# Kernel tuning notes

Measured on AMD Instinct MI355X. Metric: run time of the kernel, lower is better.

The kernel has to match this reference:

```python
import jax, jax.numpy as jnp
import numpy as np

IN_CH = 128
HID = 64
EPS = 1e-5
N_NODES = 20000
E_UND = 80000


def _build_line_graph(edge_index, num_nodes):
    # dedupe to unique undirected edges (src<dst); line-graph nodes = these edges
    src = np.asarray(edge_index[0]); dst = np.asarray(edge_index[1])
    m = src < dst
    u, v = src[m], dst[m]
    key = u.astype(np.int64) * num_nodes + v.astype(np.int64)
    _, first = np.unique(key, return_index=True)
    u, v = u[first], v[first]
    E = u.shape[0]
    # incidence lists grouped by node; all ordered pairs of co-incident edges
    nodes = np.concatenate([u, v])
    eids = np.concatenate([np.arange(E), np.arange(E)])
    order = np.argsort(nodes, kind="stable")
    nodes_s, eids_s = nodes[order], eids[order]
    counts = np.bincount(nodes_s, minlength=num_nodes)
    offsets = np.concatenate([np.zeros(1, np.int64), np.cumsum(counts)])
    grp_start = offsets[nodes_s]
    reps = counts[nodes_s]
    total = int(reps.sum())
    starts = np.cumsum(reps) - reps
    idx = np.arange(total) - np.repeat(starts, reps) + np.repeat(grp_start, reps)
    row = np.repeat(eids_s, reps); col = eids_s[idx]
    keep = row != col
    return np.stack([u, v]), np.stack([row[keep], col[keep]])


def _gcn_conv(x, src, dst, W, b):
    # PyG GCNConv: add self loops, symmetric D^-1/2 (A+I) D^-1/2 normalization
    N = x.shape[0]
    sl = jnp.arange(N)
    s = jnp.concatenate([src, sl]); d = jnp.concatenate([dst, sl])
    deg = jax.ops.segment_sum(jnp.ones(s.shape[0], x.dtype), d, num_segments=N)
    dinv = jax.lax.rsqrt(jnp.maximum(deg, 1.0))
    h = x @ W
    msg = h[s] * (dinv[s] * dinv[d])[:, None]
    return jax.ops.segment_sum(msg, d, num_segments=N) + b


def _edge_scores(line_x, lsrc, ldst, W1, b1, gamma1, beta1, W2, b2):
    h = _gcn_conv(line_x, lsrc, ldst, W1, b1)
    mu = h.mean(0); var = h.var(0)  # BatchNorm1d, training-mode batch stats
    h = jax.nn.relu(gamma1 * (h - mu) * jax.lax.rsqrt(var + EPS) + beta1)
    return jax.nn.sigmoid(_gcn_conv(h, lsrc, ldst, W2, b2))[:, 0]


def _cluster(clean, topk_idx, num_nodes):
    ti = np.asarray(topk_idx)
    sel_src = np.asarray(clean[0])[ti]; sel_dst = np.asarray(clean[1])[ti]
    n2c = np.arange(num_nodes)
    rev = sel_dst[::-1]
    _, fi = np.unique(rev, return_index=True)
    last = sel_dst.shape[0] - 1 - fi
    n2c[sel_dst[last]] = sel_src[last]
    uniq = np.unique(n2c)
    M = int(uniq.shape[0])
    old_to_new = np.full(num_nodes, -1, np.int64)
    old_to_new[uniq] = np.arange(M)
    return old_to_new[n2c], uniq, M


def _make_graph():
    rng = np.random.default_rng(0)
    a = rng.integers(0, N_NODES, E_UND)
    off = rng.integers(1, N_NODES, E_UND)
    b = (a + off) % N_NODES  # no self loops
    u = np.minimum(a, b); v = np.maximum(a, b)
    return np.stack([np.concatenate([u, v]), np.concatenate([v, u])]).astype(np.int64)


def _make_params():
    ks = jax.random.split(jax.random.key(0), 4)
    x = jax.random.normal(ks[0], (N_NODES, IN_CH), jnp.float32)
    W1 = jax.random.normal(ks[1], (IN_CH, HID), jnp.float32) / np.float32(np.sqrt(IN_CH))
    b1 = jnp.zeros((HID,), jnp.float32)
    gamma1 = jnp.ones((HID,), jnp.float32)
    beta1 = jnp.zeros((HID,), jnp.float32)
    W2 = jax.random.normal(ks[2], (HID, 1), jnp.float32) / np.float32(np.sqrt(HID))
    b2 = jnp.zeros((1,), jnp.float32)
    return x, W1, b1, gamma1, beta1, W2, b2


def setup_inputs() -> dict:
    x, W1, b1, gamma1, beta1, W2, b2 = _make_params()
    return {
        "x": x, "W1": W1, "b1": b1, "gamma1": gamma1, "beta1": beta1,
        "W2": W2, "b2": b2,
        "edge_index": jnp.asarray(_make_graph()),
        "batch": jnp.zeros((N_NODES,), jnp.int32),
    }


def reference(x, W1, b1, gamma1, beta1, W2, b2, edge_index, batch):
    N = x.shape[0]
    clean, line_ei = _build_line_graph(edge_index, N)
    csrc = jnp.asarray(clean[0]); cdst = jnp.asarray(clean[1])
    lsrc = jnp.asarray(line_ei[0]); ldst = jnp.asarray(line_ei[1])
    line_x = 0.5 * (x[csrc] + x[cdst])  # line-graph node features
    scores = _edge_scores(line_x, lsrc, ldst, W1, b1, gamma1, beta1, W2, b2)
    E_c = scores.shape[0]
    k = max(1, min(E_c // 2, N // 2))
    _, topk_idx = jax.lax.top_k(scores, k)
    new_indices, uniq, M = _cluster(clean, topk_idx, N)
    ni = jnp.asarray(new_indices)
    # aggregate: per-cluster mean of member node features (code's weights are unused)
    counts = jax.ops.segment_sum(jnp.ones(N, x.dtype), ni, num_segments=M)
    x_pool = jax.ops.segment_sum(x, ni, num_segments=M) / counts[:, None]
    batch_pool = batch[jnp.asarray(uniq)]
    # build_new_edges: relabel, drop self loops, coalesce (sorted unique)
    ei = np.asarray(edge_index)
    ns = new_indices[ei[0]]; nd = new_indices[ei[1]]
    keep = ns != nd
    pk = ns[keep] * M + nd[keep]
    upk = np.unique(pk)
    edge_index_pool = jnp.asarray(np.stack([upk // M, upk % M]))
    return (x_pool, edge_index_pool, batch_pool, scores, ni)
```

## Files before the change

kernel.cpp:

```cpp
#include <hip/hip_runtime.h>
#include <stdint.h>

typedef unsigned long long u64;
typedef unsigned int u32;

#define NND 20000
#define EUA 160000
#define EFE 80000
#define ICH 128
#define HIDC 64
#define SCAN_BS 256
#define NB_N ((NND + 255) / 256)
#define NB_EU ((EUA + 255) / 256)
#define NB_EF ((EFE + 255) / 256)
#define NB_E64 ((EFE * HIDC + 255) / 256)
#define NSCAN_B ((NND + SCAN_BS - 1) / SCAN_BS)
#define HIST_BLOCKS 128
#define GEB 64
#define XS_PAD 132
#define NCHAIN 4096
#define BK64 64
#define SEL_BINS 4096


__global__ void kScanA(const int* __restrict__ in, int* __restrict__ out,
                       int* __restrict__ bsums, int n) {
    __shared__ int sh[SCAN_BS];
    int tid = threadIdx.x;
    int i = blockIdx.x * SCAN_BS + tid;
    int v = (i < n) ? in[i] : 0;
    sh[tid] = v;
    __syncthreads();
    for (int o = 1; o < SCAN_BS; o <<= 1) {
        int t = (tid >= o) ? sh[tid - o] : 0;
        __syncthreads();
        sh[tid] += t;
        __syncthreads();
    }
    if (i < n) out[i] = sh[tid] - v;
    if (tid == SCAN_BS - 1) bsums[blockIdx.x] = sh[tid];
}
__global__ void kScanB(int* __restrict__ out, const int* __restrict__ bsums,
                       int n, int nb, int* __restrict__ totalDst) {
    __shared__ int sh[160];
    int tid = threadIdx.x;
    if (tid <= nb) sh[tid] = (tid < nb) ? bsums[tid] : 0;
    __syncthreads();
    if (tid == 0) {
        int acc = 0;
        for (int i = 0; i < nb; i++) { int t = sh[i]; sh[i] = acc; acc += t; }
        sh[nb] = acc;
    }
    __syncthreads();
    int i = blockIdx.x * SCAN_BS + tid;
    if (i < n) out[i] += sh[blockIdx.x];
    if (i == 0) {
        int tot = sh[nb];
        out[n] = tot;
        *totalDst = tot;
    }
}

__global__ void kFilterScatter64(const int* __restrict__ ei, int* __restrict__ cnt,
                                 int* __restrict__ bucketV) {
    int i = blockIdx.x * 256 + threadIdx.x;
    if (i >= EUA) return;
    int s = ei[i], d = ei[EUA + i];
    if (s < d) {
        int p = atomicAdd(&cnt[s], 1);
        bucketV[(s << 6) + p] = d;
    }
}
__global__ void kRankSort64(const int* __restrict__ in, int* __restrict__ out,
                            const int* __restrict__ lenA, int* __restrict__ ucnt) {
    int a = blockIdx.x;
    int len = lenA[a];
    int base = a << 6;
    for (int j = threadIdx.x; j < len; j += 64) {
        int v = in[base + j];
        int r = 0;
        for (int i = 0; i < len; i++) {
            int w = in[base + i];
            r += (w < v) || (w == v && i < j);
        }
        out[base + r] = v;
    }
    __syncthreads();
    int c = 0;
    for (int j = threadIdx.x; j < len; j += 64)
        c += (j == 0) || (out[base + j] != out[base + j - 1]);
#pragma unroll
    for (int o = 32; o > 0; o >>= 1) c += __shfl_down(c, o, 64);
    if (threadIdx.x == 0) ucnt[a] = c;
}
__global__ void kCompactInc(const int* __restrict__ arr, const int* __restrict__ cnt,
                            const int* __restrict__ uoff, int* __restrict__ eU,
                            int* __restrict__ eV, int* __restrict__ icnt) {
    int u = blockIdx.x * 256 + threadIdx.x;
    if (u >= NND) return;
    int s = u << 6, e = s + cnt[u], o = uoff[u];
    int myc = 0;
    for (int i = s; i < e; i++)
        if (i == s || arr[i] != arr[i - 1]) {
            int v = arr[i];
            eU[o] = u; eV[o] = v; o++;
            atomicAdd(&icnt[v], 1);
            myc++;
        }
    if (myc) atomicAdd(&icnt[u], myc);
}

__global__ void kIncScatterDinv64(const int* __restrict__ eU, const int* __restrict__ eV,
                                  const int* __restrict__ scal, int* __restrict__ itmp,
                                  int* __restrict__ ilist, const int* __restrict__ icnt,
                                  float* __restrict__ dinv) {
    int e = blockIdx.x * 256 + threadIdx.x;
    if (e >= scal[0]) return;
    int u = eU[e], v = eV[e];
    ilist[(u << 6) + atomicAdd(&itmp[u], 1)] = e;
    ilist[(v << 6) + atomicAdd(&itmp[v], 1)] = e;
    dinv[e] = rsqrtf((float)(icnt[u] + icnt[v] - 1));
}

__global__ void kGemm(const float* __restrict__ x, const float* __restrict__ W1,
                      const int* __restrict__ eU, const int* __restrict__ eV,
                      const int* __restrict__ scal, float* __restrict__ h) {
    __shared__ float W1s[ICH][HIDC];
    __shared__ float xs[GEB][XS_PAD];
    int t = threadIdx.x;
    int E = scal[0];
    int e0 = blockIdx.x * GEB;
    if (e0 >= E) return;

    {
        const float4* Wv = (const float4*)W1;
        float4* Ws = (float4*)&W1s[0][0];
        for (int i = t; i < ICH * HIDC / 4; i += 256) Ws[i] = Wv[i];
    }
    {
        int eb = t >> 2, q = t & 3;
        int e = e0 + eb;
        if (e < E) {
            int u = eU[e], v = eV[e];
            const float4* xu = (const float4*)(x + (size_t)u * ICH) + q * 8;
            const float4* xv = (const float4*)(x + (size_t)v * ICH) + q * 8;
            float* xd = &xs[eb][q * 32];
#pragma unroll
            for (int i = 0; i < 8; i++) {
                float4 a = xu[i], b = xv[i];
                xd[i * 4 + 0] = 0.5f * (a.x + b.x);
                xd[i * 4 + 1] = 0.5f * (a.y + b.y);
                xd[i * 4 + 2] = 0.5f * (a.z + b.z);
                xd[i * 4 + 3] = 0.5f * (a.w + b.w);
            }
        }
    }
    __syncthreads();

    int cg4 = (t & 15) * 4;
    int es = t >> 4;
    float a00=0,a01=0,a02=0,a03=0, a10=0,a11=0,a12=0,a13=0;
    float a20=0,a21=0,a22=0,a23=0, a30=0,a31=0,a32=0,a33=0;
#pragma unroll 4
    for (int k = 0; k < ICH; k++) {
        float4 wv = *(const float4*)&W1s[k][cg4];
        float x0 = xs[es][k], x1 = xs[es + 16][k];
        float x2 = xs[es + 32][k], x3 = xs[es + 48][k];
        a00 += x0 * wv.x; a01 += x0 * wv.y; a02 += x0 * wv.z; a03 += x0 * wv.w;
        a10 += x1 * wv.x; a11 += x1 * wv.y; a12 += x1 * wv.z; a13 += x1 * wv.w;
        a20 += x2 * wv.x; a21 += x2 * wv.y; a22 += x2 * wv.z; a23 += x2 * wv.w;
        a30 += x3 * wv.x; a31 += x3 * wv.y; a32 += x3 * wv.z; a33 += x3 * wv.w;
    }
    int e;
    e = e0 + es;
    if (e < E) *(float4*)&h[(size_t)e * HIDC + cg4] = make_float4(a00, a01, a02, a03);
    e = e0 + es + 16;
    if (e < E) *(float4*)&h[(size_t)e * HIDC + cg4] = make_float4(a10, a11, a12, a13);
    e = e0 + es + 32;
    if (e < E) *(float4*)&h[(size_t)e * HIDC + cg4] = make_float4(a20, a21, a22, a23);
    e = e0 + es + 48;
    if (e < E) *(float4*)&h[(size_t)e * HIDC + cg4] = make_float4(a30, a31, a32, a33);
}

__global__ void kSGather(const float* __restrict__ h, const float* __restrict__ dinv,
                         const int* __restrict__ icnt, const int* __restrict__ ilist,
                         float* __restrict__ S) {
    int n = blockIdx.x;
    int c = threadIdx.x;
    int base = n << 6, len = icnt[n];
    float acc = 0.f;
    for (int j = 0; j < len; j++) {
        int ed = ilist[base + j];
        acc += h[(size_t)ed * HIDC + c] * dinv[ed];
    }
    S[(size_t)n * HIDC + c] = acc;
}
__global__ void kConv1Red1(const float* __restrict__ h, const float* __restrict__ S,
                           const float* __restrict__ dinv, const int* __restrict__ eU,
                           const int* __restrict__ eV, const float* __restrict__ b1,
                           const int* __restrict__ scal, float* __restrict__ h2,
                           float* __restrict__ partial, float* __restrict__ partial2) {
    int t = threadIdx.x;
    int g = blockIdx.x * 4 + (t >> 6);
    int c = t & 63;
    int E = scal[0];
    float bc = b1[c];
    float acc = 0.f, acc2 = 0.f;
    for (int e = g; e < E; e += NCHAIN) {
        float a = dinv[e];
        float v = a * (S[(size_t)eU[e] * HIDC + c] + S[(size_t)eV[e] * HIDC + c]) -
                  a * a * h[(size_t)e * HIDC + c] + bc;
        h2[(size_t)e * HIDC + c] = v;
        acc += v;
        acc2 += v * v;
    }
    partial[g * HIDC + c] = acc;
    partial2[g * HIDC + c] = acc2;
}
__global__ void kRed2(const float* __restrict__ partial, const float* __restrict__ partial2,
                      const int* __restrict__ scal, float* __restrict__ muvar) {
    __shared__ float sh[4][HIDC];
    __shared__ float sh2[4][HIDC];
    int t = threadIdx.x;
    int q = t >> 6, c = t & 63;
    float acc = 0.f, acc2 = 0.f;
    int g0 = q * (NCHAIN / 4);
    for (int g = g0; g < g0 + NCHAIN / 4; g++) {
        acc += partial[g * HIDC + c];
        acc2 += partial2[g * HIDC + c];
    }
    sh[q][c] = acc;
    sh2[q][c] = acc2;
    __syncthreads();
    if (q == 0) {
        float Ef = (float)scal[0];
        float mu = (((sh[0][c] + sh[1][c]) + sh[2][c]) + sh[3][c]) / Ef;
        float m2 = (((sh2[0][c] + sh2[1][c]) + sh2[2][c]) + sh2[3][c]) / Ef;
        muvar[c] = mu;
        muvar[HIDC + c] = m2 - mu * mu;
    }
}
__global__ void kNormZ(const float* __restrict__ h2, const float* __restrict__ muvar,
                       const float* __restrict__ gamma1, const float* __restrict__ beta1,
                       const float* __restrict__ W2, const int* __restrict__ scal,
                       float* __restrict__ z) {
    int idx = blockIdx.x * 256 + threadIdx.x;
    int e = idx >> 6;
    if (e >= scal[0]) return;
    int c = idx & 63;
    float t = gamma1[c] * (h2[idx] - muvar[c]) * rsqrtf(muvar[HIDC + c] + 1e-5f) + beta1[c];
    t = t > 0.f ? t : 0.f;
    float p = t * W2[c];
#pragma unroll
    for (int o = 32; o > 0; o >>= 1) p += __shfl_down(p, o, 64);
    if (c == 0) z[e] = p;
}
__global__ void kS2(const float* __restrict__ z, const float* __restrict__ dinv,
                    const int* __restrict__ icnt, const int* __restrict__ ilist,
                    float* __restrict__ S2) {
    int n = blockIdx.x * 256 + threadIdx.x;
    if (n >= NND) return;
    int base = n << 6, len = icnt[n];
    float acc = 0.f;
    for (int j = 0; j < len; j++) {
        int e = ilist[base + j];
        acc += z[e] * dinv[e];
    }
    S2[n] = acc;
}
__global__ void kScore(const float* __restrict__ z, const float* __restrict__ S2,
                       const float* __restrict__ dinv, const int* __restrict__ eU,
                       const int* __restrict__ eV, const float* __restrict__ b2,
                       const int* __restrict__ scal, float* __restrict__ score,
                       u64* __restrict__ okey, u64* __restrict__ minOkey,
                       int* __restrict__ hist0) {
    __shared__ int sh[SEL_BINS];
    int t = threadIdx.x;
    for (int j = t; j < SEL_BINS; j += 256) sh[j] = 0;
    __syncthreads();
    int e = blockIdx.x * 256 + t;
    if (e < NND) minOkey[e] = ~0ULL;
    int E = scal[0];
    if (e < E) {
        float a = dinv[e];
        float l = a * (S2[eU[e]] + S2[eV[e]]) - a * a * z[e] + b2[0];
        float s = 1.f / (1.f + expf(-l));
        score[e] = s;
        u32 b = __float_as_uint(s);
        b = (b >> 31) ? ~b : (b | 0x80000000u);
        u64 key = (((u64)b) << 17) | (u32)(0x1FFFFu - (u32)e);
        okey[e] = key;
        atomicAdd(&sh[(int)((key >> 36) & (SEL_BINS - 1))], 1);
    }
    __syncthreads();
    for (int j = t; j < SEL_BINS; j += 256) {
        int v = sh[j];
        if (v) atomicAdd(&hist0[j], v);
    }
}

__device__ __forceinline__ u64 selReplay(const int* __restrict__ histBase, int passes,
                                         int E, int t, int* aux, int* shTmp) {
    int kr = E / 2;
    if (kr > NND / 2) kr = NND / 2;
    if (kr < 1) kr = 1;
    u64 pref = 1ULL << 48;
    for (int q = 0; q < passes; q++) {
        int shift = 36 - 12 * q;
        const int* hq = histBase + q * SEL_BINS;
        int b[16];
        int g = 0;
#pragma unroll
        for (int j = 0; j < 16; j++) { b[j] = hq[16 * t + j]; g += b[j]; }
        aux[t] = g;
        __syncthreads();
        for (int o = 1; o < 256; o <<= 1) {
            int v = (t + o < 256) ? aux[t + o] : 0;
            __syncthreads();
            aux[t] += v;
            __syncthreads();
        }
        int suf = aux[t] - g;
        if (suf < kr && kr <= suf + g) {
            int cum = suf, found = 16 * t;
            for (int j = 15; j >= 0; j--) {
                int hc = b[j];
                if (cum + hc >= kr) { found = 16 * t + j; break; }
                cum += hc;
            }
            shTmp[0] = found;
            shTmp[1] = kr - cum;
        }
        __syncthreads();
        pref |= ((u64)shTmp[0]) << shift;
        kr = shTmp[1];
        __syncthreads();
    }
    return pref;
}
__global__ void kHistR(const u64* __restrict__ okey, const int* __restrict__ scal,
                       int* __restrict__ histBase, int pass) {
    __shared__ int sh[4][SEL_BINS];
    __shared__ int aux[256];
    __shared__ int shTmp[2];
    int t = threadIdx.x;
    int E = scal[0];
    u64 p = selReplay(histBase, pass, E, t, aux, shTmp);
    for (int j = t; j < 4 * SEL_BINS; j += 256) ((int*)sh)[j] = 0;
    __syncthreads();
    int wv = t >> 6;
    int shift = 36 - 12 * pass;
    u64 maskHi = (~0ULL) << (shift + 12);
    for (int e = blockIdx.x * 256 + t; e < E; e += HIST_BLOCKS * 256) {
        u64 kk = okey[e];
        if ((kk & maskHi) == p)
            atomicAdd(&sh[wv][(int)((kk >> shift) & (SEL_BINS - 1))], 1);
    }
    __syncthreads();
    int* hp = histBase + pass * SEL_BINS;
    for (int j = t; j < SEL_BINS; j += 256) {
        int v = sh[0][j] + sh[1][j] + sh[2][j] + sh[3][j];
        if (v) atomicAdd(&hp[j], v);
    }
}

__global__ void kMinKey(const u64* __restrict__ okey, const int* __restrict__ eV,
                        const int* __restrict__ scal, const int* __restrict__ histBase,
                        u64* __restrict__ minOkey) {
    __shared__ int aux[256];
    __shared__ int shTmp[2];
    int t = threadIdx.x;
    int E = scal[0];
    u64 pref = selReplay(histBase, 4, E, t, aux, shTmp);
    int i = blockIdx.x * 256 + t;
    if (i < E) {
        u64 k = okey[i];
        if (k >= pref) atomicMin(&minOkey[eV[i]], k);
    }
}
__global__ void kCluster(const u64* __restrict__ minOkey, const int* __restrict__ eU,
                         int* __restrict__ n2c, int* __restrict__ present,
                         int* __restrict__ csize, int* __restrict__ cmemb) {
    int v = blockIdx.x * 256 + threadIdx.x;
    if (v >= NND) return;
    u64 mk = minOkey[v];
    int m = v;
    if (mk != ~0ULL) m = eU[0x1FFFFu - (u32)(mk & 0x1FFFFu)];
    n2c[v] = m;
    present[m] = 1;
    int slot = atomicAdd(&csize[m], 1);
    cmemb[(m << 6) + slot] = v;
}

__global__ void kXPoolCE(const float* __restrict__ x, const int* __restrict__ n2c,
                         const int* __restrict__ o2n, const int* __restrict__ present,
                         const int* __restrict__ csize, const int* __restrict__ cmemb,
                         const int* __restrict__ ei, int* __restrict__ ni,
                         float* __restrict__ dout, int* __restrict__ ecnt2) {
    int u = blockIdx.x;
    int c = threadIdx.x;
    int gid = u * 128 + c;
    if (gid < EUA) {
        int a = o2n[n2c[ei[gid]]], b = o2n[n2c[ei[EUA + gid]]];
        if (a != b) atomicAdd(&ecnt2[a], 1);
    }
    if (c == 0) ni[u] = o2n[n2c[u]];
    if (!present[u]) return;
    int s = csize[u];
    int base = u << 6;
    float acc = 0.f;
    for (int j = 0; j < s; j++)
        acc += x[(size_t)cmemb[base + j] * ICH + c];
    dout[(size_t)o2n[u] * ICH + c] = acc / (float)s;
}

__global__ void kCEscatter(const int* __restrict__ ei, const int* __restrict__ ni,
                           const int* __restrict__ eoff2, int* __restrict__ etmp2,
                           int* __restrict__ bkD) {
    int i = blockIdx.x * 256 + threadIdx.x;
    if (i >= EUA) return;
    int a = ni[ei[i]], b = ni[ei[EUA + i]];
    if (a != b) {
        int p = eoff2[a] + atomicAdd(&etmp2[a], 1);
        bkD[p] = b;
    }
}
__global__ void kRankSort(const int* __restrict__ in, int* __restrict__ out,
                          const int* __restrict__ offA, int* __restrict__ ucnt) {
    int a = blockIdx.x;
    int s = offA[a], e = offA[a + 1], len = e - s;
    for (int j = threadIdx.x; j < len; j += 64) {
        int v = in[s + j];
        int r = 0;
        for (int i = 0; i < len; i++) {
            int w = in[s + i];
            r += (w < v) || (w == v && i < j);
        }
        out[s + r] = v;
    }
    __syncthreads();
    int c = 0;
    for (int j = threadIdx.x; j < len; j += 64)
        c += (j == 0) || (out[s + j] != out[s + j - 1]);
#pragma unroll
    for (int o = 32; o > 0; o >>= 1) c += __shfl_down(c, o, 64);
    if (threadIdx.x == 0) ucnt[a] = c;
}
__global__ void kCEwriteTail(const int* __restrict__ bkD2, const int* __restrict__ eoff2,
                             const int* __restrict__ ueoff, const int* __restrict__ scal,
                             const int* __restrict__ batch, const int* __restrict__ present,
                             const int* __restrict__ o2n, const float* __restrict__ score,
                             const int* __restrict__ ni, float* __restrict__ dout) {
    int i = blockIdx.x * 256 + threadIdx.x;
    int E = scal[0], M = scal[2], Ep = scal[3];
    size_t base = (size_t)M * ICH;
    if (i < NND) {
        int s = eoff2[i], e = eoff2[i + 1];
        float* r0 = dout + base;
        float* r1 = r0 + Ep;
        int o = ueoff[i];
        for (int j = s; j < e; j++)
            if (j == s || bkD2[j] != bkD2[j - 1]) {
                r0[o] = (float)i;
                r1[o] = (float)bkD2[j];
                o++;
            }
    }
    size_t tb = base + 2 * (size_t)Ep;
    if (i < NND && present[i]) dout[tb + o2n[i]] = (float)batch[i];
    if (i < E) dout[tb + M + i] = score[i];
    if (i < NND) dout[tb + M + E + i] = (float)ni[i];
}

extern "C" void kernel_launch(void* const* d_in, const int* in_sizes, int n_in,
                              void* d_out, int out_size, void* d_ws, size_t ws_size,
                              hipStream_t stream) {
    (void)in_sizes; (void)n_in; (void)ws_size; (void)out_size;
    const float* x = (const float*)d_in[0];
    const float* W1 = (const float*)d_in[1];
    const float* b1 = (const float*)d_in[2];
    const float* gamma1 = (const float*)d_in[3];
    const float* beta1 = (const float*)d_in[4];
    const float* W2 = (const float*)d_in[5];
    const float* b2 = (const float*)d_in[6];
    const int* ei = (const int*)d_in[7];
    const int* batch = (const int*)d_in[8];
    float* dout = (float*)d_out;

    char* w = (char*)d_ws;
    size_t off = 0;
    auto carve = [&](size_t bytes) -> void* {
        off = (off + 255) & ~(size_t)255;
        void* p = w + off;
        off += bytes;
        return p;
    };
    char* zero0 = w;
    int* cnt = (int*)carve(NND * 4);
    int* itmp = (int*)carve(NND * 4);
    int* icnt = (int*)carve(NND * 4);
    int* present = (int*)carve(NND * 4);
    int* csize = (int*)carve(NND * 4);
    int* ecnt2 = (int*)carve(NND * 4);
    int* etmp2 = (int*)carve(NND * 4);
    int* scal = (int*)carve(16 * 4);
    int* hist4 = (int*)carve((size_t)4 * SEL_BINS * 4);
    size_t zeroBytes = off;
    int* ucnt = (int*)carve(NND * 4);
    int* uoff = (int*)carve((NND + 2) * 4);
    int* bsums = (int*)carve((NSCAN_B + 2) * 4);
    int* n2c = (int*)carve(NND * 4);
    int* o2n = (int*)carve((NND + 2) * 4);
    int* niArr = (int*)carve(NND * 4);
    int* eoff2 = (int*)carve((NND + 2) * 4);
    int* uecnt = (int*)carve(NND * 4);
    int* ueoff = (int*)carve((NND + 2) * 4);
    int* bucketV = (int*)carve((size_t)NND * BK64 * 4);
    int* bucketS = (int*)carve((size_t)NND * BK64 * 4);
    int* eU = (int*)carve(EFE * 4);
    int* eV = (int*)carve(EFE * 4);
    int* ilist = (int*)carve((size_t)NND * BK64 * 4);
    int* ilistS = (int*)carve((size_t)NND * BK64 * 4);
    int* bkD = (int*)carve(EUA * 4);
    int* bkD2 = (int*)carve(EUA * 4);
    u64* okey = (u64*)carve(EFE * 8);
    u64* minOkey = (u64*)carve(NND * 8);
    float* dinv = (float*)carve(EFE * 4);
    float* h = (float*)carve((size_t)EFE * HIDC * 4);
    float* h2 = (float*)carve((size_t)EFE * HIDC * 4);
    float* Snode = (float*)carve((size_t)NND * HIDC * 4);
    float* partial = (float*)carve((size_t)NCHAIN * HIDC * 4);
    float* partial2 = (float*)carve((size_t)NCHAIN * HIDC * 4);
    float* muvar = (float*)carve(128 * 4);
    float* zArr = (float*)carve(EFE * 4);
    float* S2 = (float*)carve(NND * 4);
    float* score = (float*)carve(EFE * 4);

    auto scan = [&](const int* in, int* outp, int* totalDst) {
        kScanA<<<NSCAN_B, SCAN_BS, 0, stream>>>(in, outp, bsums, NND);
        kScanB<<<NSCAN_B, SCAN_BS, 0, stream>>>(outp, bsums, NND, NSCAN_B, totalDst);
    };

    hipMemsetAsync(zero0, 0, zeroBytes, stream);

    kFilterScatter64<<<NB_EU, 256, 0, stream>>>(ei, cnt, bucketV);
    kRankSort64<<<NND, 64, 0, stream>>>(bucketV, bucketS, cnt, ucnt);
    scan(ucnt, uoff, scal + 0);
    kCompactInc<<<NB_N, 256, 0, stream>>>(bucketS, cnt, uoff, eU, eV, icnt);

    kIncScatterDinv64<<<NB_EF, 256, 0, stream>>>(eU, eV, scal, itmp, ilist, icnt, dinv);
    kRankSort64<<<NND, 64, 0, stream>>>(ilist, ilistS, icnt, ucnt);

    kGemm<<<(EFE + GEB - 1) / GEB, 256, 0, stream>>>(x, W1, eU, eV, scal, h);
    kSGather<<<NND, HIDC, 0, stream>>>(h, dinv, icnt, ilistS, Snode);
    kConv1Red1<<<NCHAIN / 4, 256, 0, stream>>>(h, Snode, dinv, eU, eV, b1, scal, h2,
                                               partial, partial2);
    kRed2<<<1, 256, 0, stream>>>(partial, partial2, scal, muvar);
    kNormZ<<<NB_E64, 256, 0, stream>>>(h2, muvar, gamma1, beta1, W2, scal, zArr);

    kS2<<<NB_N, 256, 0, stream>>>(zArr, dinv, icnt, ilistS, S2);
    kScore<<<NB_EF, 256, 0, stream>>>(zArr, S2, dinv, eU, eV, b2, scal, score, okey,
                                      minOkey, hist4);

    for (int p = 1; p < 4; p++)
        kHistR<<<HIST_BLOCKS, 256, 0, stream>>>(okey, scal, hist4, p);

    kMinKey<<<NB_EF, 256, 0, stream>>>(okey, eV, scal, hist4, minOkey);
    kCluster<<<NB_N, 256, 0, stream>>>(minOkey, eU, n2c, present, csize, bucketV);
    scan(present, o2n, scal + 2);

    kXPoolCE<<<NND, 128, 0, stream>>>(x, n2c, o2n, present, csize, bucketV, ei,
                                      niArr, dout, ecnt2);

    scan(ecnt2, eoff2, scal + 4);
    kCEscatter<<<NB_EU, 256, 0, stream>>>(ei, niArr, eoff2, etmp2, bkD);
    kRankSort<<<NND, 64, 0, stream>>>(bkD, bkD2, eoff2, uecnt);
    scan(uecnt, ueoff, scal + 3);
    kCEwriteTail<<<NB_EF, 256, 0, stream>>>(bkD2, eoff2, ueoff, scal, batch, present,
                                            o2n, score, niArr, dout);
}
```

Baseline: 360.4 us.

## Fuse mid-pipeline GCN, batchnorm, scoring and top-k selection into one persistent kernel

Result: slower. 834.0 us (+131.4%).

```diff
diff --git a/kernel.cpp b/kernel.cpp
--- a/kernel.cpp
+++ b/kernel.cpp
@@ -13,14 +13,14 @@
 #define NB_N ((NND + 255) / 256)
 #define NB_EU ((EUA + 255) / 256)
 #define NB_EF ((EFE + 255) / 256)
-#define NB_E64 ((EFE * HIDC + 255) / 256)
 #define NSCAN_B ((NND + SCAN_BS - 1) / SCAN_BS)
-#define HIST_BLOCKS 128
 #define GEB 64
 #define XS_PAD 132
-#define NCHAIN 4096
 #define BK64 64
 #define SEL_BINS 4096
+#define FBLK 512
+#define CHAINS 4096
+#define VMAX ((EFE + CHAINS - 1) / CHAINS)
 
 
 __global__ void kScanA(const int* __restrict__ in, int* __restrict__ out,
@@ -182,123 +182,6 @@
     if (e < E) *(float4*)&h[(size_t)e * HIDC + cg4] = make_float4(a30, a31, a32, a33);
 }
 
-__global__ void kSGather(const float* __restrict__ h, const float* __restrict__ dinv,
-                         const int* __restrict__ icnt, const int* __restrict__ ilist,
-                         float* __restrict__ S) {
-    int n = blockIdx.x;
-    int c = threadIdx.x;
-    int base = n << 6, len = icnt[n];
-    float acc = 0.f;
-    for (int j = 0; j < len; j++) {
-        int ed = ilist[base + j];
-        acc += h[(size_t)ed * HIDC + c] * dinv[ed];
-    }
-    S[(size_t)n * HIDC + c] = acc;
-}
-__global__ void kConv1Red1(const float* __restrict__ h, const float* __restrict__ S,
-                           const float* __restrict__ dinv, const int* __restrict__ eU,
-                           const int* __restrict__ eV, const float* __restrict__ b1,
-                           const int* __restrict__ scal, float* __restrict__ h2,
-                           float* __restrict__ partial, float* __restrict__ partial2) {
-    int t = threadIdx.x;
-    int g = blockIdx.x * 4 + (t >> 6);
-    int c = t & 63;
-    int E = scal[0];
-    float bc = b1[c];
-    float acc = 0.f, acc2 = 0.f;
-    for (int e = g; e < E; e += NCHAIN) {
-        float a = dinv[e];
-        float v = a * (S[(size_t)eU[e] * HIDC + c] + S[(size_t)eV[e] * HIDC + c]) -
-                  a * a * h[(size_t)e * HIDC + c] + bc;
-        h2[(size_t)e * HIDC + c] = v;
-        acc += v;
-        acc2 += v * v;
-    }
-    partial[g * HIDC + c] = acc;
-    partial2[g * HIDC + c] = acc2;
-}
-__global__ void kRed2(const float* __restrict__ partial, const float* __restrict__ partial2,
-                      const int* __restrict__ scal, float* __restrict__ muvar) {
-    __shared__ float sh[4][HIDC];
-    __shared__ float sh2[4][HIDC];
-    int t = threadIdx.x;
-    int q = t >> 6, c = t & 63;
-    float acc = 0.f, acc2 = 0.f;
-    int g0 = q * (NCHAIN / 4);
-    for (int g = g0; g < g0 + NCHAIN / 4; g++) {
-        acc += partial[g * HIDC + c];
-        acc2 += partial2[g * HIDC + c];
-    }
-    sh[q][c] = acc;
-    sh2[q][c] = acc2;
-    __syncthreads();
-    if (q == 0) {
-        float Ef = (float)scal[0];
-        float mu = (((sh[0][c] + sh[1][c]) + sh[2][c]) + sh[3][c]) / Ef;
-        float m2 = (((sh2[0][c] + sh2[1][c]) + sh2[2][c]) + sh2[3][c]) / Ef;
-        muvar[c] = mu;
-        muvar[HIDC + c] = m2 - mu * mu;
-    }
-}
-__global__ void kNormZ(const float* __restrict__ h2, const float* __restrict__ muvar,
-                       const float* __restrict__ gamma1, const float* __restrict__ beta1,
-                       const float* __restrict__ W2, const int* __restrict__ scal,
-                       float* __restrict__ z) {
-    int idx = blockIdx.x * 256 + threadIdx.x;
-    int e = idx >> 6;
-    if (e >= scal[0]) return;
-    int c = idx & 63;
-    float t = gamma1[c] * (h2[idx] - muvar[c]) * rsqrtf(muvar[HIDC + c] + 1e-5f) + beta1[c];
-    t = t > 0.f ? t : 0.f;
-    float p = t * W2[c];
-#pragma unroll
-    for (int o = 32; o > 0; o >>= 1) p += __shfl_down(p, o, 64);
-    if (c == 0) z[e] = p;
-}
-__global__ void kS2(const float* __restrict__ z, const float* __restrict__ dinv,
-                    const int* __restrict__ icnt, const int* __restrict__ ilist,
-                    float* __restrict__ S2) {
-    int n = blockIdx.x * 256 + threadIdx.x;
-    if (n >= NND) return;
-    int base = n << 6, len = icnt[n];
-    float acc = 0.f;
-    for (int j = 0; j < len; j++) {
-        int e = ilist[base + j];
-        acc += z[e] * dinv[e];
-    }
-    S2[n] = acc;
-}
-__global__ void kScore(const float* __restrict__ z, const float* __restrict__ S2,
-                       const float* __restrict__ dinv, const int* __restrict__ eU,
-                       const int* __restrict__ eV, const float* __restrict__ b2,
-                       const int* __restrict__ scal, float* __restrict__ score,
-                       u64* __restrict__ okey, u64* __restrict__ minOkey,
-                       int* __restrict__ hist0) {
-    __shared__ int sh[SEL_BINS];
-    int t = threadIdx.x;
-    for (int j = t; j < SEL_BINS; j += 256) sh[j] = 0;
-    __syncthreads();
-    int e = blockIdx.x * 256 + t;
-    if (e < NND) minOkey[e] = ~0ULL;
-    int E = scal[0];
-    if (e < E) {
-        float a = dinv[e];
-        float l = a * (S2[eU[e]] + S2[eV[e]]) - a * a * z[e] + b2[0];
-        float s = 1.f / (1.f + expf(-l));
-        score[e] = s;
-        u32 b = __float_as_uint(s);
-        b = (b >> 31) ? ~b : (b | 0x80000000u);
-        u64 key = (((u64)b) << 17) | (u32)(0x1FFFFu - (u32)e);
-        okey[e] = key;
-        atomicAdd(&sh[(int)((key >> 36) & (SEL_BINS - 1))], 1);
-    }
-    __syncthreads();
-    for (int j = t; j < SEL_BINS; j += 256) {
-        int v = sh[j];
-        if (v) atomicAdd(&hist0[j], v);
-    }
-}
-
 __device__ __forceinline__ u64 selReplay(const int* __restrict__ histBase, int passes,
                                          int E, int t, int* aux, int* shTmp) {
     int kr = E / 2;
@@ -338,58 +221,202 @@
     }
     return pref;
 }
-__global__ void kHistR(const u64* __restrict__ okey, const int* __restrict__ scal,
-                       int* __restrict__ histBase, int pass) {
-    __shared__ int sh[4][SEL_BINS];
+
+__device__ __forceinline__ void gsync(int* bar, int target) {
+    __syncthreads();
+    if (threadIdx.x == 0) {
+        __threadfence();
+        atomicAdd(bar, 1);
+        while (atomicAdd(bar, 0) < target)
+            __builtin_amdgcn_s_sleep(2);
+        __threadfence();
+    }
+    __syncthreads();
+}
+
+struct FParams {
+    const float* h; const float* dinv; const int* icnt; const int* ilistS;
+    const int* eU; const int* eV;
+    const float* b1; const float* gamma1; const float* beta1;
+    const float* W2; const float* b2;
+    const int* scal;
+    float* Snode; float* partial; float* partial2; float* miniP;
+    float* z; float* S2; float* score;
+    u64* okey; u64* minOkey; int* hist;
+    int* n2c; int* present; int* csize; int* cmemb;
+    int* bar;
+};
+
+__global__ __launch_bounds__(256, 2) void kFusedMid(FParams P) {
+    __shared__ int shHist[SEL_BINS];
     __shared__ int aux[256];
     __shared__ int shTmp[2];
     int t = threadIdx.x;
-    int E = scal[0];
-    u64 p = selReplay(histBase, pass, E, t, aux, shTmp);
-    for (int j = t; j < 4 * SEL_BINS; j += 256) ((int*)sh)[j] = 0;
-    __syncthreads();
-    int wv = t >> 6;
-    int shift = 36 - 12 * pass;
-    u64 maskHi = (~0ULL) << (shift + 12);
-    for (int e = blockIdx.x * 256 + t; e < E; e += HIST_BLOCKS * 256) {
-        u64 kk = okey[e];
-        if ((kk & maskHi) == p)
-            atomicAdd(&sh[wv][(int)((kk >> shift) & (SEL_BINS - 1))], 1);
-    }
-    __syncthreads();
-    int* hp = histBase + pass * SEL_BINS;
+    int b = blockIdx.x;
+    int gtid = b * 256 + t;
+    int w = t >> 6, c = t & 63;
+    int E = P.scal[0];
+    int barPhase = 0;
+#define GSYNC() do { barPhase += FBLK; gsync(P.bar, barPhase); } while (0)
+
+    for (int id = gtid; id < NND * HIDC; id += FBLK * 256) {
+        int n = id >> 6;
+        int base = n << 6, len = P.icnt[n];
+        float acc = 0.f;
+        for (int j = 0; j < len; j++) {
+            int ed = P.ilistS[base + j];
+            acc += P.h[(size_t)ed * HIDC + c] * P.dinv[ed];
+        }
+        P.Snode[id] = acc;
+    }
+    GSYNC();
+
+    int gw = b * 4 + w;
+    int cA = 2 * gw, cB = cA + 1;
+    float vA[VMAX], vB[VMAX];
+    {
+        float bc = P.b1[c];
+        float accA = 0.f, acc2A = 0.f, accB = 0.f, acc2B = 0.f;
+#pragma unroll
+        for (int it = 0; it < VMAX; it++) {
+            int eA = cA + it * CHAINS;
+            if (eA < E) {
+                float a = P.dinv[eA];
+                float val = a * (P.Snode[(size_t)P.eU[eA] * HIDC + c] +
+                                 P.Snode[(size_t)P.eV[eA] * HIDC + c]) -
+                            a * a * P.h[(size_t)eA * HIDC + c] + bc;
+                vA[it] = val; accA += val; acc2A += val * val;
+            } else vA[it] = 0.f;
+            int eB = cB + it * CHAINS;
+            if (eB < E) {
+                float a = P.dinv[eB];
+                float val = a * (P.Snode[(size_t)P.eU[eB] * HIDC + c] +
+                                 P.Snode[(size_t)P.eV[eB] * HIDC + c]) -
+                            a * a * P.h[(size_t)eB * HIDC + c] + bc;
+                vB[it] = val; accB += val; acc2B += val * val;
+            } else vB[it] = 0.f;
+        }
+        P.partial [cA * HIDC + c] = accA;
+        P.partial2[cA * HIDC + c] = acc2A;
+        P.partial [cB * HIDC + c] = accB;
+        P.partial2[cB * HIDC + c] = acc2B;
+    }
+    GSYNC();
+
+    if (b < 8 && t < HIDC) {
+        int q = b & 3;
+        const float* src = ((b & 4) ? P.partial2 : P.partial) +
+                           (size_t)q * (CHAINS / 4) * HIDC + t;
+        float acc = 0.f;
+        for (int r = 0; r < CHAINS / 4; r++) acc += src[(size_t)r * HIDC];
+        P.miniP[b * HIDC + t] = acc;
+    }
+    GSYNC();
+
+    {
+        float Ef = (float)E;
+        float mu = (((P.miniP[0 * HIDC + c] + P.miniP[1 * HIDC + c]) +
+                     P.miniP[2 * HIDC + c]) + P.miniP[3 * HIDC + c]) / Ef;
+        float m2 = (((P.miniP[4 * HIDC + c] + P.miniP[5 * HIDC + c]) +
+                     P.miniP[6 * HIDC + c]) + P.miniP[7 * HIDC + c]) / Ef;
+        float rs = rsqrtf(m2 - mu * mu + 1e-5f);
+        float gc = P.gamma1[c], be = P.beta1[c], wc = P.W2[c];
+#pragma unroll
+        for (int it = 0; it < VMAX; it++) {
+            int eA = cA + it * CHAINS;
+            if (eA < E) {
+                float tt = gc * (vA[it] - mu) * rs + be;
+                tt = tt > 0.f ? tt : 0.f;
+                float p = tt * wc;
+#pragma unroll
+                for (int o = 32; o > 0; o >>= 1) p += __shfl_down(p, o, 64);
+                if (c == 0) P.z[eA] = p;
+            }
+            int eB = cB + it * CHAINS;
+            if (eB < E) {
+                float tt = gc * (vB[it] - mu) * rs + be;
+                tt = tt > 0.f ? tt : 0.f;
+                float p = tt * wc;
+#pragma unroll
+                for (int o = 32; o > 0; o >>= 1) p += __shfl_down(p, o, 64);
+                if (c == 0) P.z[eB] = p;
+            }
+        }
+    }
+    GSYNC();
+
+    if (gtid < NND) {
+        int base = gtid << 6, len = P.icnt[gtid];
+        float a3 = 0.f;
+        for (int j = 0; j < len; j++) {
+            int e = P.ilistS[base + j];
+            a3 += P.z[e] * P.dinv[e];
+        }
+        P.S2[gtid] = a3;
+        P.minOkey[gtid] = ~0ULL;
+    }
+    GSYNC();
+
+    for (int j = t; j < SEL_BINS; j += 256) shHist[j] = 0;
+    __syncthreads();
+    if (gtid < E) {
+        float a = P.dinv[gtid];
+        float l = a * (P.S2[P.eU[gtid]] + P.S2[P.eV[gtid]]) - a * a * P.z[gtid] +
+                  P.b2[0];
+        float s = 1.f / (1.f + expf(-l));
+        P.score[gtid] = s;
+        u32 bb = __float_as_uint(s);
+        bb = (bb >> 31) ? ~bb : (bb | 0x80000000u);
+        u64 key = (((u64)bb) << 17) | (u32)(0x1FFFFu - (u32)gtid);
+        P.okey[gtid] = key;
+        atomicAdd(&shHist[(int)((key >> 36) & (SEL_BINS - 1))], 1);
+    }
+    __syncthreads();
     for (int j = t; j < SEL_BINS; j += 256) {
-        int v = sh[0][j] + sh[1][j] + sh[2][j] + sh[3][j];
-        if (v) atomicAdd(&hp[j], v);
-    }
-}
-
-__global__ void kMinKey(const u64* __restrict__ okey, const int* __restrict__ eV,
-                        const int* __restrict__ scal, const int* __restrict__ histBase,
-                        u64* __restrict__ minOkey) {
-    __shared__ int aux[256];
-    __shared__ int shTmp[2];
-    int t = threadIdx.x;
-    int E = scal[0];
-    u64 pref = selReplay(histBase, 4, E, t, aux, shTmp);
-    int i = blockIdx.x * 256 + t;
-    if (i < E) {
-        u64 k = okey[i];
-        if (k >= pref) atomicMin(&minOkey[eV[i]], k);
-    }
-}
-__global__ void kCluster(const u64* __restrict__ minOkey, const int* __restrict__ eU,
-                         int* __restrict__ n2c, int* __restrict__ present,
-                         int* __restrict__ csize, int* __restrict__ cmemb) {
-    int v = blockIdx.x * 256 + threadIdx.x;
-    if (v >= NND) return;
-    u64 mk = minOkey[v];
-    int m = v;
-    if (mk != ~0ULL) m = eU[0x1FFFFu - (u32)(mk & 0x1FFFFu)];
-    n2c[v] = m;
-    present[m] = 1;
-    int slot = atomicAdd(&csize[m], 1);
-    cmemb[(m << 6) + slot] = v;
+        int vv = shHist[j];
+        if (vv) atomicAdd(&P.hist[j], vv);
+    }
+    GSYNC();
+
+    for (int pass = 1; pass < 4; pass++) {
+        u64 pref = selReplay(P.hist, pass, E, t, aux, shTmp);
+        for (int j = t; j < SEL_BINS; j += 256) shHist[j] = 0;
+        __syncthreads();
+        int shift = 36 - 12 * pass;
+        u64 maskHi = (~0ULL) << (shift + 12);
+        if (gtid < E) {
+            u64 kk = P.okey[gtid];
+            if ((kk & maskHi) == pref)
+                atomicAdd(&shHist[(int)((kk >> shift) & (SEL_BINS - 1))], 1);
+        }
+        __syncthreads();
+        int* hp = P.hist + pass * SEL_BINS;
+        for (int j = t; j < SEL_BINS; j += 256) {
+            int vv = shHist[j];
+            if (vv) atomicAdd(&hp[j], vv);
+        }
+        GSYNC();
+    }
+
+    {
+        u64 pref = selReplay(P.hist, 4, E, t, aux, shTmp);
+        if (gtid < E) {
+            u64 k = P.okey[gtid];
+            if (k >= pref) atomicMin(&P.minOkey[P.eV[gtid]], k);
+        }
+    }
+    GSYNC();
+
+    if (gtid < NND) {
+        u64 mk = P.minOkey[gtid];
+        int m = gtid;
+        if (mk != ~0ULL) m = P.eU[0x1FFFFu - (u32)(mk & 0x1FFFFu)];
+        P.n2c[gtid] = m;
+        P.present[m] = 1;
+        int slot = atomicAdd(&P.csize[m], 1);
+        P.cmemb[(m << 6) + slot] = gtid;
+    }
+#undef GSYNC
 }
 
 __global__ void kXPoolCE(const float* __restrict__ x, const int* __restrict__ n2c,
@@ -505,6 +532,7 @@
     int* etmp2 = (int*)carve(NND * 4);
     int* scal = (int*)carve(16 * 4);
     int* hist4 = (int*)carve((size_t)4 * SEL_BINS * 4);
+    int* gbar = (int*)carve(64 * 4);
     size_t zeroBytes = off;
     int* ucnt = (int*)carve(NND * 4);
     int* uoff = (int*)carve((NND + 2) * 4);
@@ -527,11 +555,10 @@
     u64* minOkey = (u64*)carve(NND * 8);
     float* dinv = (float*)carve(EFE * 4);
     float* h = (float*)carve((size_t)EFE * HIDC * 4);
-    float* h2 = (float*)carve((size_t)EFE * HIDC * 4);
     float* Snode = (float*)carve((size_t)NND * HIDC * 4);
-    float* partial = (float*)carve((size_t)NCHAIN * HIDC * 4);
-    float* partial2 = (float*)carve((size_t)NCHAIN * HIDC * 4);
-    float* muvar = (float*)carve(128 * 4);
+    float* partial = (float*)carve((size_t)CHAINS * HIDC * 4);
+    float* partial2 = (float*)carve((size_t)CHAINS * HIDC * 4);
+    float* miniP = (float*)carve(8 * HIDC * 4);
     float* zArr = (float*)carve(EFE * 4);
     float* S2 = (float*)carve(NND * 4);
     float* score = (float*)carve(EFE * 4);
@@ -552,21 +579,19 @@
     kRankSort64<<<NND, 64, 0, stream>>>(ilist, ilistS, icnt, ucnt);
 
     kGemm<<<(EFE + GEB - 1) / GEB, 256, 0, stream>>>(x, W1, eU, eV, scal, h);
-    kSGather<<<NND, HIDC, 0, stream>>>(h, dinv, icnt, ilistS, Snode);
-    kConv1Red1<<<NCHAIN / 4, 256, 0, stream>>>(h, Snode, dinv, eU, eV, b1, scal, h2,
-                                               partial, partial2);
-    kRed2<<<1, 256, 0, stream>>>(partial, partial2, scal, muvar);
-    kNormZ<<<NB_E64, 256, 0, stream>>>(h2, muvar, gamma1, beta1, W2, scal, zArr);
-
-    kS2<<<NB_N, 256, 0, stream>>>(zArr, dinv, icnt, ilistS, S2);
-    kScore<<<NB_EF, 256, 0, stream>>>(zArr, S2, dinv, eU, eV, b2, scal, score, okey,
-                                      minOkey, hist4);
-
-    for (int p = 1; p < 4; p++)
-        kHistR<<<HIST_BLOCKS, 256, 0, stream>>>(okey, scal, hist4, p);
-
-    kMinKey<<<NB_EF, 256, 0, stream>>>(okey, eV, scal, hist4, minOkey);
-    kCluster<<<NB_N, 256, 0, stream>>>(minOkey, eU, n2c, present, csize, bucketV);
+
+    FParams fp;
+    fp.h = h; fp.dinv = dinv; fp.icnt = icnt; fp.ilistS = ilistS;
+    fp.eU = eU; fp.eV = eV;
+    fp.b1 = b1; fp.gamma1 = gamma1; fp.beta1 = beta1; fp.W2 = W2; fp.b2 = b2;
+    fp.scal = scal;
+    fp.Snode = Snode; fp.partial = partial; fp.partial2 = partial2; fp.miniP = miniP;
+    fp.z = zArr; fp.S2 = S2; fp.score = score;
+    fp.okey = okey; fp.minOkey = minOkey; fp.hist = hist4;
+    fp.n2c = n2c; fp.present = present; fp.csize = csize; fp.cmemb = bucketV;
+    fp.bar = gbar;
+    kFusedMid<<<FBLK, 256, 0, stream>>>(fp);
+
     scan(present, o2n, scal + 2);
 
     kXPoolCE<<<NND, 128, 0, stream>>>(x, n2c, o2n, present, csize, bucketV, ei,
```
